# Kernel optimization log

Measured on AMD Instinct MI355X. Metric: run time of the kernel, lower is better.

Reference implementation:

```python
import jax, jax.numpy as jnp
import numpy as np

B, S, HN, TN = 8, 32, 64, 512
HID, EMB, VOCAB = 512, 512, 10000


def setup_inputs():
    key = jax.random.key(0)
    k = jax.random.split(key, 14)
    w = lambda kk, shape: jax.random.normal(kk, shape, jnp.float32) * 0.02
    return {
        "dec_out": jax.random.normal(k[0], (B, S, HID), jnp.float32),
        "history": jax.random.normal(k[1], (B, HID), jnp.float32),
        "head": jax.random.randint(k[2], (B, HN), 0, VOCAB),
        "tail": jax.random.randint(k[3], (B, TN), 0, VOCAB),
        "adj_mask": jax.random.randint(k[4], (B, HN, TN), 0, 2).astype(bool),
        "dup_mask": jax.random.randint(k[5], (B, S, TN), 0, 2).astype(bool),
        "emb_table": w(k[6], (VOCAB, EMB)),
        "W_tq": w(k[7], (2 * HID + EMB, HID)),
        "b_tq": jnp.zeros((HID,), jnp.float32),
        "W_tk": w(k[8], (EMB, HID)),
        "b_tk": jnp.zeros((HID,), jnp.float32),
        "W_tout": w(k[9], (2 * HID, HID)),
        "W_hq": w(k[10], (2 * HID, HID)),
        "b_hq": jnp.zeros((HID,), jnp.float32),
        "W_hk": w(k[11], (HID, HID)),
        "b_hk": jnp.zeros((HID,), jnp.float32),
    }


def reference(dec_out, history, head, tail, adj_mask, dup_mask, emb_table,
              W_tq, b_tq, W_tk, b_tk, W_tout, W_hq, b_hq, W_hk, b_hk):
    head_emb = emb_table[head]  # (B, HN, EMB)
    tail_emb = emb_table[tail]  # (B, TN, EMB)

    # --- tail attention query: Linear(cat([dec_out, history, head_emb])) + ELU.
    # Same math as the torch broadcast-concat, computed as a sum of three
    # partial matmuls to avoid materializing the (B,S,HN,2*hid+emb) concat.
    Wd, Wh, We = W_tq[:HID], W_tq[HID:2 * HID], W_tq[2 * HID:]
    tq = jax.nn.elu((dec_out @ Wd)[:, :, None, :]
                    + (history @ Wh)[:, None, None, :]
                    + (head_emb @ We)[:, None, :, :]
                    + b_tq)                       # (B, S, HN, HID)
    tq = tq.reshape(B, S * HN, HID)
    tk = jax.nn.elu(tail_emb @ W_tk + b_tk)       # (B, TN, HID)  (dropout=eval)

    # combined logical mask: allowed = adjacency AND not-duplicate
    mask = (adj_mask[:, None, :, :] & ~dup_mask[:, :, None, :]).reshape(B, S * HN, TN)

    # GlobalAttention (dot): score -> mask -> softmax -> context -> tanh(linear_out([c;q]))
    scores = jnp.einsum('bqh,bth->bqt', tq, tk)   # (B, S*HN, TN)
    tail_attn = jax.nn.softmax(jnp.where(mask, scores, -jnp.inf), axis=-1)
    ctx = jnp.einsum('bqt,bth->bqh', tail_attn, tk)
    graph_hid = jnp.tanh(ctx @ W_tout[:HID] + tq @ W_tout[HID:])
    graph_hid = graph_hid.reshape(B * S, HN, HID)
    tail_attn = tail_attn.reshape(B * S, HN, TN)

    # --- head attention (one-step), length-masked over HN
    hq = jax.nn.elu(dec_out @ W_hq[:HID] + (history @ W_hq[HID:])[:, None, :] + b_hq)
    hq = hq.reshape(B * S, HID)
    hk = jax.nn.elu(jnp.einsum('nkh,hd->nkd', graph_hid, W_hk) + b_hk)
    lengths = jnp.repeat(jnp.sum(head != 0, axis=-1), S)          # (B*S,)
    hscores = jnp.einsum('nh,nkh->nk', hq, hk)                    # (B*S, HN)
    lmask = jnp.arange(HN)[None, :] < lengths[:, None]
    head_attn = jax.nn.softmax(jnp.where(lmask, hscores, -jnp.inf), axis=-1)
    # (head-attention context output is discarded by the original module)

    prob = jnp.einsum('nk,nkt->nt', head_attn, tail_attn).reshape(B, S, TN)
    return jnp.log(prob + 1e-20)
```

## Files before the change

kernel.cpp:

```cpp
#include <hip/hip_runtime.h>
#include <math.h>

#define BB 8
#define SS 32
#define HN 64
#define TN 512
#define HID 512

typedef __attribute__((ext_vector_type(8))) short short8;
typedef __attribute__((ext_vector_type(4))) float f32x4;

__device__ __forceinline__ float eluf(float x) { return x > 0.f ? x : (expf(x) - 1.f); }

__device__ __forceinline__ short f2bs(float f) {
    union { float f; unsigned int u; } v; v.f = f;
    unsigned int r = v.u + 0x7fffu + ((v.u >> 16) & 1u);
    return (short)(r >> 16);
}
__device__ __forceinline__ float b2f(short s) {
    union { unsigned int u; float f; } v;
    v.u = ((unsigned int)(unsigned short)s) << 16;
    return v.f;
}

__device__ __forceinline__ void gld16(const void* g, void* l) {
    __builtin_amdgcn_global_load_lds(
        (const __attribute__((address_space(1))) void*)g,
        (__attribute__((address_space(3))) void*)l, 16, 0, 0);
}

template <int ACT, int OUTB, int DUAL>
__device__ __forceinline__ void gcore(
    const short* __restrict__ A, const short* __restrict__ B,
    const short* __restrict__ A2, const short* __restrict__ B2,
    const float* __restrict__ bias, void* __restrict__ Cv,
    int ldc, int K, int m0, int n0, int cm0, short* Ls,
    const float* __restrict__ hq, float* __restrict__ hsp)
{
    short* Al = Ls;
    short* Bl = Ls + 8192;
    const int tid  = threadIdx.x;
    const int lane = tid & 63;
    const int w    = tid >> 6;
    const int wr   = w >> 1, wc = w & 1;
    const int l16  = lane & 15, quad = lane >> 4;

    const int srow = w * 16 + (lane >> 2);
    const int scol = (lane & 3) * 8;

    f32x4 acc[4][4];
#pragma unroll
    for (int i = 0; i < 4; ++i)
#pragma unroll
        for (int j = 0; j < 4; ++j) { acc[i][j][0]=0.f; acc[i][j][1]=0.f; acc[i][j][2]=0.f; acc[i][j][3]=0.f; }

    short* lA = Al + w * 512;
    short* lB = Bl + w * 512;
    const long rstep = (long)64 * K;

    for (int rep = 0; rep <= DUAL; ++rep) {
        const short* Ag = (rep ? A2 : A) + (long)(m0 + srow) * K + scol;
        const short* Bg = (rep ? B2 : B) + (long)(n0 + srow) * K + scol;
        for (int kt = 0; kt < K; kt += 64) {
            __syncthreads();
            gld16(Ag + kt, lA);
            gld16(Ag + kt + rstep, lA + 2048);
            gld16(Ag + kt + 32, lA + 4096);
            gld16(Ag + kt + 32 + rstep, lA + 4096 + 2048);
            gld16(Bg + kt, lB);
            gld16(Bg + kt + rstep, lB + 2048);
            gld16(Bg + kt + 32, lB + 4096);
            gld16(Bg + kt + 32 + rstep, lB + 4096 + 2048);
            __syncthreads();
#pragma unroll
            for (int h = 0; h < 2; ++h) {
                short8 af[4], bf4[4];
#pragma unroll
                for (int mi = 0; mi < 4; ++mi)
                    af[mi] = *(const short8*)(Al + h * 4096 + (wr * 64 + mi * 16 + l16) * 32 + quad * 8);
#pragma unroll
                for (int ni = 0; ni < 4; ++ni)
                    bf4[ni] = *(const short8*)(Bl + h * 4096 + (wc * 64 + ni * 16 + l16) * 32 + quad * 8);
#pragma unroll
                for (int mi = 0; mi < 4; ++mi)
#pragma unroll
                    for (int ni = 0; ni < 4; ++ni)
                        acc[mi][ni] = __builtin_amdgcn_mfma_f32_16x16x32_bf16(af[mi], bf4[ni], acc[mi][ni], 0, 0, 0);
            }
        }
    }

    __syncthreads();

    float bv[4];
#pragma unroll
    for (int ni = 0; ni < 4; ++ni)
        bv[ni] = bias ? bias[n0 + wc * 64 + ni * 16 + l16] : 0.f;

    if (OUTB == 1) {
        short* eb = Ls + w * 1152;
        const int er = lane >> 2;
        const int ec = (lane & 3) * 16;
#pragma unroll
        for (int mi = 0; mi < 4; ++mi) {
#pragma unroll
            for (int ni = 0; ni < 4; ++ni)
#pragma unroll
                for (int r = 0; r < 4; ++r) {
                    float x = acc[mi][ni][r] + bv[ni];
                    if (ACT == 1) x = eluf(x);
                    else if (ACT == 2) x = tanhf(x);
                    eb[(quad * 4 + r) * 72 + ni * 16 + l16] = f2bs(x);
                }
            __builtin_amdgcn_sched_barrier(0);
            short8 v0 = *(const short8*)&eb[er * 72 + ec];
            short8 v1 = *(const short8*)&eb[er * 72 + ec + 8];
            long cb = (long)(cm0 + wr * 64 + mi * 16 + er) * ldc + n0 + wc * 64 + ec;
            *(short8*)((short*)Cv + cb)     = v0;
            *(short8*)((short*)Cv + cb + 8) = v1;
            __builtin_amdgcn_sched_barrier(0);
        }
    } else if (OUTB == 2) {
        const int n_w = (cm0 + wr * 64) >> 6;
        float hqv[4];
#pragma unroll
        for (int ni = 0; ni < 4; ++ni)
            hqv[ni] = hq[(long)n_w * 512 + n0 + wc * 64 + ni * 16 + l16];
        float* red = (float*)Ls;
#pragma unroll
        for (int mi = 0; mi < 4; ++mi)
#pragma unroll
            for (int r = 0; r < 4; ++r) {
                float p = 0.f;
#pragma unroll
                for (int ni = 0; ni < 4; ++ni) {
                    float x = acc[mi][ni][r] + bv[ni];
                    if (ACT == 1) x = eluf(x);
                    p += x * hqv[ni];
                }
                p += __shfl_xor(p, 1);
                p += __shfl_xor(p, 2);
                p += __shfl_xor(p, 4);
                p += __shfl_xor(p, 8);
                if (l16 == 0) red[w * 64 + mi * 16 + quad * 4 + r] = p;
            }
        __syncthreads();
        if (tid < 128) {
            int wr2 = tid >> 6, rw = tid & 63;
            float v = red[(wr2 * 2 + 0) * 64 + rw] + red[(wr2 * 2 + 1) * 64 + rw];
            hsp[(long)(n0 >> 7) * 16384 + cm0 + tid] = v;
        }
    } else {
#pragma unroll
        for (int mi = 0; mi < 4; ++mi)
#pragma unroll
            for (int ni = 0; ni < 4; ++ni) {
                int gc = n0 + wc * 64 + ni * 16 + l16;
#pragma unroll
                for (int r = 0; r < 4; ++r) {
                    float x = acc[mi][ni][r] + bv[ni];
                    if (ACT == 1) x = eluf(x);
                    else if (ACT == 2) x = tanhf(x);
                    ((float*)Cv)[(long)(cm0 + wr * 64 + mi * 16 + quad * 4 + r) * ldc + gc] = x;
                }
            }
    }
}

template <int ACT, int OUTB, int DUAL>
__global__ __launch_bounds__(256) void mgemm(
    const short* __restrict__ A, long sAz,
    const short* __restrict__ B, long sBz,
    const short* __restrict__ A2, long sA2z,
    const short* __restrict__ B2,
    const float* __restrict__ bias,
    void* __restrict__ Cv, long sCz, int ldc, int K)
{
    __shared__ short Ls[16384];
    const int z = blockIdx.z;
    void* C = OUTB ? (void*)((short*)Cv + (long)z * sCz) : (void*)((float*)Cv + (long)z * sCz);
    const short* A2z = DUAL ? (A2 + (long)z * sA2z) : nullptr;
    gcore<ACT, OUTB, DUAL>(A + (long)z * sAz, B + (long)z * sBz, A2z, B2, bias, C,
                           ldc, K, blockIdx.y * 128, blockIdx.x * 128, blockIdx.y * 128, Ls,
                           nullptr, nullptr);
}

__global__ __launch_bounds__(256) void mgemm_hs(
    const short* __restrict__ A, const short* __restrict__ B,
    const float* __restrict__ bias, const float* __restrict__ hq, float* __restrict__ hsp)
{
    __shared__ short Ls[16384];
    gcore<1, 2, 0>(A, B, nullptr, nullptr, bias, nullptr, 512, 512,
                   blockIdx.y * 128, blockIdx.x * 128, blockIdx.y * 128, Ls, hq, hsp);
}

__global__ __launch_bounds__(256) void mgemm_multi(
    const short* __restrict__ decb, const short* __restrict__ WTall, float* __restrict__ qall,
    const short* __restrict__ embAll, const short* __restrict__ WTe, float* __restrict__ qe,
    const short* __restrict__ WTk, const float* __restrict__ b_tk, short* __restrict__ tkb)
{
    __shared__ short Ls[16384];
    int id = blockIdx.x;
    if (id < 48) {
        int y = id >> 4, x = id & 15;
        gcore<0, 0, 0>(decb, WTall, nullptr, nullptr, nullptr, qall, 2048, 512,
                       y * 128, x * 128, y * 128, Ls, nullptr, nullptr);
    } else if (id < 64) {
        int id2 = id - 48, y = id2 >> 2, x = id2 & 3;
        gcore<0, 0, 0>(embAll, WTe, nullptr, nullptr, nullptr, qe, 512, 512,
                       y * 128, x * 128, y * 128, Ls, nullptr, nullptr);
    } else {
        int id3 = id - 64, y = id3 >> 2, x = id3 & 3;
        gcore<1, 1, 0>(embAll, WTk, nullptr, nullptr, b_tk, tkb, 512, 512,
                       512 + y * 128, x * 128, y * 128, Ls, nullptr, nullptr);
    }
}

struct WTDesc { const float* src[9]; short* dst[9]; };

__global__ __launch_bounds__(256) void prep(
    const float* __restrict__ dec_out, const float* __restrict__ history,
    short* __restrict__ decb,
    const float* __restrict__ emb, const int* __restrict__ head, const int* __restrict__ tail,
    short* __restrict__ embAll, WTDesc wd)
{
    __shared__ float t[32][33];
    const int id = blockIdx.x, tid = threadIdx.x;
    if (id < 528) {
        int i = id * 256 + tid;
        float v = (i < 131072) ? dec_out[i] : history[i - 131072];
        decb[i] = f2bs(v);
    } else if (id < 528 + 4608) {
        int r = id - 528;
        int idx = (r < 512) ? head[r] : tail[r - 512];
        const float* s = emb + (long)idx * 512;
        short* dst = embAll + (long)r * 512;
        dst[tid]       = f2bs(s[tid]);
        dst[tid + 256] = f2bs(s[tid + 256]);
    } else {
        int q = id - 5136;
        int z = q >> 8, xy = q & 255;
        int x = xy & 15, y = xy >> 4;
        const float* src = wd.src[z];
        short* dst = wd.dst[z];
        int k0 = y * 32, n0 = x * 32;
        int tx = tid & 31, ty = tid >> 5;
#pragma unroll
        for (int i = 0; i < 32; i += 8)
            t[ty + i][tx] = src[(long)(k0 + ty + i) * 512 + n0 + tx];
        __syncthreads();
#pragma unroll
        for (int i = 0; i < 32; i += 8)
            dst[(long)(n0 + ty + i) * 512 + k0 + tx] = f2bs(t[tx][ty + i]);
    }
}

__global__ __launch_bounds__(256) void l3_kernel(
    const float* __restrict__ qall, const float* __restrict__ qe,
    const float* __restrict__ b_tq, short* __restrict__ tqb,
    const short* __restrict__ WTo1, const short* __restrict__ tkb, short* __restrict__ tkWTb,
    const float* __restrict__ b_hq, float* __restrict__ hqf)
{
    __shared__ short Ls[16384];
    if (blockIdx.x < 8192) {
        long gid = (long)blockIdx.x * 256 + threadIdx.x;
        int r = (int)(gid >> 7), j0 = ((int)gid & 127) * 4;
        int b = r >> 11, rem = r & 2047, s = rem >> 6, h = rem & 63;
        float4 d = *(const float4*)(qall + (long)(b * 32 + s) * 2048 + j0);
        float4 q = *(const float4*)(qall + (long)(256 + b) * 2048 + 1024 + j0);
        float4 e = *(const float4*)(qe + (long)(b * 64 + h) * 512 + j0);
        float4 bb = *(const float4*)(b_tq + j0);
        short4 o;
        o.x = f2bs(eluf(d.x + q.x + e.x + bb.x));
        o.y = f2bs(eluf(d.y + q.y + e.y + bb.y));
        o.z = f2bs(eluf(d.z + q.z + e.z + bb.z));
        o.w = f2bs(eluf(d.w + q.w + e.w + bb.w));
        *(short4*)(tqb + (long)r * 512 + j0) = o;
    } else if (blockIdx.x < 8320) {
        int id2 = blockIdx.x - 8192;
        int z = id2 >> 4, r = id2 & 15;
        int x = r & 3, y = r >> 2;
        gcore<0, 1, 0>(WTo1, tkb + (long)z * 262144, nullptr, nullptr, nullptr,
                       tkWTb + (long)z * 262144, 512, 512, y * 128, x * 128, y * 128, Ls,
                       nullptr, nullptr);
    } else {
        long gid = (long)(blockIdx.x - 8320) * 256 + threadIdx.x;
        int n = (int)(gid >> 7), j0 = ((int)gid & 127) * 4;
        int b = n >> 5;
        float4 d = *(const float4*)(qall + (long)n * 2048 + 512 + j0);
        float4 h2 = *(const float4*)(qall + (long)(256 + b) * 2048 + 1536 + j0);
        float4 bb = *(const float4*)(b_hq + j0);
        float4 o;
        o.x = eluf(d.x + h2.x + bb.x);
        o.y = eluf(d.y + h2.y + bb.y);
        o.z = eluf(d.z + h2.z + bb.z);
        o.w = eluf(d.w + h2.w + bb.w);
        *(float4*)(hqf + (long)n * 512 + j0) = o;
    }
}

__global__ __launch_bounds__(256) void sm_kernel(
    const short* __restrict__ sc, const int* __restrict__ adj, const int* __restrict__ dup,
    short* __restrict__ Pb)
{
    int w = threadIdx.x >> 6, lane = threadIdx.x & 63;
    long r = (long)blockIdx.x * 4 + w;
    int b = (int)(r >> 11), rem = (int)(r & 2047), s = rem >> 6, h = rem & 63;
    const short* row = sc + r * 512 + lane * 8;
    const int* adjr = adj + ((long)(b * 64 + h)) * 512 + lane * 8;
    const int* dupr = dup + ((long)(b * 32 + s)) * 512 + lane * 8;
    short8 v8 = *(const short8*)row;
    int4 a0 = *(const int4*)adjr, a1 = *(const int4*)(adjr + 4);
    int4 d0 = *(const int4*)dupr, d1 = *(const int4*)(dupr + 4);
    int am[8] = {a0.x, a0.y, a0.z, a0.w, a1.x, a1.y, a1.z, a1.w};
    int dm[8] = {d0.x, d0.y, d0.z, d0.w, d1.x, d1.y, d1.z, d1.w};
    float v[8];
    float m = -INFINITY;
#pragma unroll
    for (int i = 0; i < 8; ++i) {
        v[i] = (am[i] && !dm[i]) ? b2f(v8[i]) : -INFINITY;
        m = fmaxf(m, v[i]);
    }
#pragma unroll
    for (int d = 32; d >= 1; d >>= 1) m = fmaxf(m, __shfl_xor(m, d));
    float sum = 0.f;
#pragma unroll
    for (int i = 0; i < 8; ++i) {
        float e = (m == -INFINITY) ? 0.f : expf(v[i] - m);
        v[i] = e; sum += e;
    }
#pragma unroll
    for (int d = 32; d >= 1; d >>= 1) sum += __shfl_xor(sum, d);
    float inv = sum > 0.f ? 1.f / sum : 0.f;
    short8 o;
#pragma unroll
    for (int i = 0; i < 8; ++i) o[i] = f2bs(v[i] * inv);
    *(short8*)(Pb + r * 512 + lane * 8) = o;
}

__global__ __launch_bounds__(256) void fused_head(
    const float* __restrict__ hsp, const int* __restrict__ head,
    const short* __restrict__ ta, float* __restrict__ out)
{
    int n = blockIdx.x, b = n >> 5;
    int tid = threadIdx.x;
    __shared__ float hal[64];
    __shared__ float part[4][512];

    if (tid < 64) {
        float sv_raw = hsp[n * 64 + tid] + hsp[16384 + n * 64 + tid]
                     + hsp[2 * 16384 + n * 64 + tid] + hsp[3 * 16384 + n * 64 + tid];
        int hv = head[b * 64 + tid];
        unsigned long long ball = __ballot(hv != 0);
        int len = __popcll(ball);
        float sv = (tid < len) ? sv_raw : -INFINITY;
        float m = sv;
#pragma unroll
        for (int d = 32; d >= 1; d >>= 1) m = fmaxf(m, __shfl_xor(m, d));
        float e = expf(sv - m);
        float sum = e;
#pragma unroll
        for (int d = 32; d >= 1; d >>= 1) sum += __shfl_xor(sum, d);
        hal[tid] = e / sum;
    }
    __syncthreads();

    {
        int w = tid >> 6, lane = tid & 63;
        const short* tab = ta + (long)n * 64 * 512 + (long)(w * 16) * 512 + lane * 8;
        float acc[8] = {};
#pragma unroll
        for (int k = 0; k < 16; ++k) {
            float a = hal[w * 16 + k];
            short8 tv = *(const short8*)(tab + (long)k * 512);
#pragma unroll
            for (int u = 0; u < 8; ++u) acc[u] += a * b2f(tv[u]);
        }
        float4* pp = (float4*)&part[w][lane * 8];
        pp[0] = make_float4(acc[0], acc[1], acc[2], acc[3]);
        pp[1] = make_float4(acc[4], acc[5], acc[6], acc[7]);
    }
    __syncthreads();

    for (int t = tid; t < 512; t += 256) {
        float a = part[0][t] + part[1][t] + part[2][t] + part[3][t];
        out[(long)n * 512 + t] = logf(a + 1e-20f);
    }
}

extern "C" void kernel_launch(void* const* d_in, const int* in_sizes, int n_in,
                              void* d_out, int out_size, void* d_ws, size_t ws_size,
                              hipStream_t stream)
{
    const float* dec_out = (const float*)d_in[0];
    const float* history = (const float*)d_in[1];
    const int*   head    = (const int*)d_in[2];
    const int*   tail    = (const int*)d_in[3];
    const int*   adj     = (const int*)d_in[4];
    const int*   dup     = (const int*)d_in[5];
    const float* emb     = (const float*)d_in[6];
    const float* W_tq    = (const float*)d_in[7];
    const float* b_tq    = (const float*)d_in[8];
    const float* W_tk    = (const float*)d_in[9];
    const float* b_tk    = (const float*)d_in[10];
    const float* W_tout  = (const float*)d_in[11];
    const float* W_hq    = (const float*)d_in[12];
    const float* b_hq    = (const float*)d_in[13];
    const float* W_hk    = (const float*)d_in[14];
    const float* b_hk    = (const float*)d_in[15];
    float* out = (float*)d_out;

    char* ws = (char*)d_ws;
    auto alloc = [&](size_t bytes) -> void* {
        char* p = ws;
        ws += (bytes + 255) & ~(size_t)255;
        return (void*)p;
    };
    short* decb   = (short*)alloc((size_t)384 * 512 * 2);
    short* embAll = (short*)alloc((size_t)4608 * 512 * 2);
    short* WT     = (short*)alloc((size_t)9 * 512 * 512 * 2);
    float* qall   = (float*)alloc((size_t)384 * 2048 * 4);
    float* qe     = (float*)alloc((size_t)512 * 512 * 4);
    float* hqf    = (float*)alloc((size_t)256 * 512 * 4);
    float* hsp    = (float*)alloc((size_t)4 * 16384 * 4);
    short* tkb    = (short*)alloc((size_t)4096 * 512 * 2);
    short* tkWTb  = (short*)alloc((size_t)4096 * 512 * 2);
    short* tqb    = (short*)alloc((size_t)16384 * 512 * 2);
    short* scb    = (short*)alloc((size_t)16384 * 512 * 2);
    short* Pb     = (short*)alloc((size_t)16384 * 512 * 2);
    short* ghb = scb;

    WTDesc wd;
    wd.src[0] = W_tq;               wd.dst[0] = WT;
    wd.src[1] = W_hq;               wd.dst[1] = WT + (size_t)1 * 262144;
    wd.src[2] = W_tq + 512 * 512;   wd.dst[2] = WT + (size_t)2 * 262144;
    wd.src[3] = W_hq + 512 * 512;   wd.dst[3] = WT + (size_t)3 * 262144;
    wd.src[4] = W_tq + 1024 * 512;  wd.dst[4] = WT + (size_t)4 * 262144;
    wd.src[5] = W_tk;               wd.dst[5] = WT + (size_t)5 * 262144;
    wd.src[6] = W_tout;             wd.dst[6] = WT + (size_t)6 * 262144;
    wd.src[7] = W_tout + 512 * 512; wd.dst[7] = WT + (size_t)7 * 262144;
    wd.src[8] = W_hk;               wd.dst[8] = WT + (size_t)8 * 262144;

    prep<<<7440, 256, 0, stream>>>(dec_out, history, decb, emb, head, tail, embAll, wd);
    mgemm_multi<<<192, 256, 0, stream>>>(decb, WT, qall, embAll, WT + (size_t)4 * 262144, qe,
                                         WT + (size_t)5 * 262144, b_tk, tkb);
    l3_kernel<<<8448, 256, 0, stream>>>(qall, qe, b_tq, tqb, WT + (size_t)6 * 262144, tkb, tkWTb,
                                        b_hq, hqf);
    mgemm<0, 1, 0><<<dim3(4, 16, 8), 256, 0, stream>>>(
        tqb, (long)2048 * 512, tkb, 262144, nullptr, 0, nullptr, nullptr,
        scb, (long)2048 * 512, 512, 512);
    sm_kernel<<<4096, 256, 0, stream>>>(scb, adj, dup, Pb);
    mgemm<2, 1, 1><<<dim3(4, 16, 8), 256, 0, stream>>>(
        Pb, (long)2048 * 512, tkWTb, 262144, tqb, (long)2048 * 512, WT + (size_t)7 * 262144,
        nullptr, ghb, (long)2048 * 512, 512, 512);
    mgemm_hs<<<dim3(4, 128), 256, 0, stream>>>(ghb, WT + (size_t)8 * 262144, b_hk, hqf, hsp);
    fused_head<<<256, 256, 0, stream>>>(hsp, head, Pb, out);
}
```

Measured before the change: 224.4 us.

## Shrink GEMM tiles to 64x128 with two-wave blocks to double grid size

The shared GEMM core changes from a 128x128 tile computed by four waves to a 64x128 tile computed by two waves, each wave owning a 64x64 sub-tile. Block size drops to 128 threads, LDS use drops to 24KB, and every GEMM launch grid doubles, along with the element-wise part of l3_kernel. The goal is more blocks and better CU occupancy on the small GEMMs (e.g. 192 or 512 blocks on a large GPU). In exchange, B-tile reuse per block falls and global loads per FLOP rise.

Result: slower. 238.2 us (+6.2%).

```diff
diff --git a/kernel.cpp b/kernel.cpp
--- a/kernel.cpp
+++ b/kernel.cpp
@@ -30,7 +30,7 @@
 }
 
 template <int ACT, int OUTB, int DUAL>
-__device__ __forceinline__ void gcore(
+__device__ __forceinline__ void gcore2(
     const short* __restrict__ A, const short* __restrict__ B,
     const short* __restrict__ A2, const short* __restrict__ B2,
     const float* __restrict__ bias, void* __restrict__ Cv,
@@ -38,11 +38,10 @@
     const float* __restrict__ hq, float* __restrict__ hsp)
 {
     short* Al = Ls;
-    short* Bl = Ls + 8192;
+    short* Bl = Ls + 4096;
     const int tid  = threadIdx.x;
     const int lane = tid & 63;
     const int w    = tid >> 6;
-    const int wr   = w >> 1, wc = w & 1;
     const int l16  = lane & 15, quad = lane >> 4;
 
     const int srow = w * 16 + (lane >> 2);
@@ -54,33 +53,36 @@
 #pragma unroll
         for (int j = 0; j < 4; ++j) { acc[i][j][0]=0.f; acc[i][j][1]=0.f; acc[i][j][2]=0.f; acc[i][j][3]=0.f; }
 
-    short* lA = Al + w * 512;
-    short* lB = Bl + w * 512;
-    const long rstep = (long)64 * K;
+    const int wb = w * 16;
+    const long r32 = (long)32 * K;
 
     for (int rep = 0; rep <= DUAL; ++rep) {
         const short* Ag = (rep ? A2 : A) + (long)(m0 + srow) * K + scol;
         const short* Bg = (rep ? B2 : B) + (long)(n0 + srow) * K + scol;
         for (int kt = 0; kt < K; kt += 64) {
             __syncthreads();
-            gld16(Ag + kt, lA);
-            gld16(Ag + kt + rstep, lA + 2048);
-            gld16(Ag + kt + 32, lA + 4096);
-            gld16(Ag + kt + 32 + rstep, lA + 4096 + 2048);
-            gld16(Bg + kt, lB);
-            gld16(Bg + kt + rstep, lB + 2048);
-            gld16(Bg + kt + 32, lB + 4096);
-            gld16(Bg + kt + 32 + rstep, lB + 4096 + 2048);
+            gld16(Ag + kt,            Al + (wb) * 32);
+            gld16(Ag + kt + r32,      Al + (wb + 32) * 32);
+            gld16(Ag + kt + 32,       Al + 2048 + (wb) * 32);
+            gld16(Ag + kt + r32 + 32, Al + 2048 + (wb + 32) * 32);
+            gld16(Bg + kt,                Bl + (wb) * 32);
+            gld16(Bg + kt + r32,          Bl + (wb + 32) * 32);
+            gld16(Bg + kt + 2 * r32,      Bl + (wb + 64) * 32);
+            gld16(Bg + kt + 3 * r32,      Bl + (wb + 96) * 32);
+            gld16(Bg + kt + 32,           Bl + 4096 + (wb) * 32);
+            gld16(Bg + kt + r32 + 32,     Bl + 4096 + (wb + 32) * 32);
+            gld16(Bg + kt + 2 * r32 + 32, Bl + 4096 + (wb + 64) * 32);
+            gld16(Bg + kt + 3 * r32 + 32, Bl + 4096 + (wb + 96) * 32);
             __syncthreads();
 #pragma unroll
             for (int h = 0; h < 2; ++h) {
                 short8 af[4], bf4[4];
 #pragma unroll
                 for (int mi = 0; mi < 4; ++mi)
-                    af[mi] = *(const short8*)(Al + h * 4096 + (wr * 64 + mi * 16 + l16) * 32 + quad * 8);
+                    af[mi] = *(const short8*)(Al + h * 2048 + (mi * 16 + l16) * 32 + quad * 8);
 #pragma unroll
                 for (int ni = 0; ni < 4; ++ni)
-                    bf4[ni] = *(const short8*)(Bl + h * 4096 + (wc * 64 + ni * 16 + l16) * 32 + quad * 8);
+                    bf4[ni] = *(const short8*)(Bl + h * 4096 + (w * 64 + ni * 16 + l16) * 32 + quad * 8);
 #pragma unroll
                 for (int mi = 0; mi < 4; ++mi)
 #pragma unroll
@@ -95,7 +97,7 @@
     float bv[4];
 #pragma unroll
     for (int ni = 0; ni < 4; ++ni)
-        bv[ni] = bias ? bias[n0 + wc * 64 + ni * 16 + l16] : 0.f;
+        bv[ni] = bias ? bias[n0 + w * 64 + ni * 16 + l16] : 0.f;
 
     if (OUTB == 1) {
         short* eb = Ls + w * 1152;
@@ -115,17 +117,17 @@
             __builtin_amdgcn_sched_barrier(0);
             short8 v0 = *(const short8*)&eb[er * 72 + ec];
             short8 v1 = *(const short8*)&eb[er * 72 + ec + 8];
-            long cb = (long)(cm0 + wr * 64 + mi * 16 + er) * ldc + n0 + wc * 64 + ec;
+            long cb = (long)(cm0 + mi * 16 + er) * ldc + n0 + w * 64 + ec;
             *(short8*)((short*)Cv + cb)     = v0;
             *(short8*)((short*)Cv + cb + 8) = v1;
             __builtin_amdgcn_sched_barrier(0);
         }
     } else if (OUTB == 2) {
-        const int n_w = (cm0 + wr * 64) >> 6;
+        const int n_w = cm0 >> 6;
         float hqv[4];
 #pragma unroll
         for (int ni = 0; ni < 4; ++ni)
-            hqv[ni] = hq[(long)n_w * 512 + n0 + wc * 64 + ni * 16 + l16];
+            hqv[ni] = hq[(long)n_w * 512 + n0 + w * 64 + ni * 16 + l16];
         float* red = (float*)Ls;
 #pragma unroll
         for (int mi = 0; mi < 4; ++mi)
@@ -145,30 +147,27 @@
                 if (l16 == 0) red[w * 64 + mi * 16 + quad * 4 + r] = p;
             }
         __syncthreads();
-        if (tid < 128) {
-            int wr2 = tid >> 6, rw = tid & 63;
-            float v = red[(wr2 * 2 + 0) * 64 + rw] + red[(wr2 * 2 + 1) * 64 + rw];
-            hsp[(long)(n0 >> 7) * 16384 + cm0 + tid] = v;
-        }
+        if (tid < 64)
+            hsp[(long)(n0 >> 7) * 16384 + cm0 + tid] = red[tid] + red[64 + tid];
     } else {
 #pragma unroll
         for (int mi = 0; mi < 4; ++mi)
 #pragma unroll
             for (int ni = 0; ni < 4; ++ni) {
-                int gc = n0 + wc * 64 + ni * 16 + l16;
+                int gc = n0 + w * 64 + ni * 16 + l16;
 #pragma unroll
                 for (int r = 0; r < 4; ++r) {
                     float x = acc[mi][ni][r] + bv[ni];
                     if (ACT == 1) x = eluf(x);
                     else if (ACT == 2) x = tanhf(x);
-                    ((float*)Cv)[(long)(cm0 + wr * 64 + mi * 16 + quad * 4 + r) * ldc + gc] = x;
+                    ((float*)Cv)[(long)(cm0 + mi * 16 + quad * 4 + r) * ldc + gc] = x;
                 }
             }
     }
 }
 
 template <int ACT, int OUTB, int DUAL>
-__global__ __launch_bounds__(256) void mgemm(
+__global__ __launch_bounds__(128) void mgemm(
     const short* __restrict__ A, long sAz,
     const short* __restrict__ B, long sBz,
     const short* __restrict__ A2, long sA2z,
@@ -176,43 +175,43 @@
     const float* __restrict__ bias,
     void* __restrict__ Cv, long sCz, int ldc, int K)
 {
-    __shared__ short Ls[16384];
+    __shared__ short Ls[12288];
     const int z = blockIdx.z;
     void* C = OUTB ? (void*)((short*)Cv + (long)z * sCz) : (void*)((float*)Cv + (long)z * sCz);
     const short* A2z = DUAL ? (A2 + (long)z * sA2z) : nullptr;
-    gcore<ACT, OUTB, DUAL>(A + (long)z * sAz, B + (long)z * sBz, A2z, B2, bias, C,
-                           ldc, K, blockIdx.y * 128, blockIdx.x * 128, blockIdx.y * 128, Ls,
-                           nullptr, nullptr);
-}
-
-__global__ __launch_bounds__(256) void mgemm_hs(
+    gcore2<ACT, OUTB, DUAL>(A + (long)z * sAz, B + (long)z * sBz, A2z, B2, bias, C,
+                            ldc, K, blockIdx.y * 64, blockIdx.x * 128, blockIdx.y * 64, Ls,
+                            nullptr, nullptr);
+}
+
+__global__ __launch_bounds__(128) void mgemm_hs(
     const short* __restrict__ A, const short* __restrict__ B,
     const float* __restrict__ bias, const float* __restrict__ hq, float* __restrict__ hsp)
 {
-    __shared__ short Ls[16384];
-    gcore<1, 2, 0>(A, B, nullptr, nullptr, bias, nullptr, 512, 512,
-                   blockIdx.y * 128, blockIdx.x * 128, blockIdx.y * 128, Ls, hq, hsp);
-}
-
-__global__ __launch_bounds__(256) void mgemm_multi(
+    __shared__ short Ls[12288];
+    gcore2<1, 2, 0>(A, B, nullptr, nullptr, bias, nullptr, 512, 512,
+                    blockIdx.y * 64, blockIdx.x * 128, blockIdx.y * 64, Ls, hq, hsp);
+}
+
+__global__ __launch_bounds__(128) void mgemm_multi(
     const short* __restrict__ decb, const short* __restrict__ WTall, float* __restrict__ qall,
     const short* __restrict__ embAll, const short* __restrict__ WTe, float* __restrict__ qe,
     const short* __restrict__ WTk, const float* __restrict__ b_tk, short* __restrict__ tkb)
 {
-    __shared__ short Ls[16384];
+    __shared__ short Ls[12288];
     int id = blockIdx.x;
-    if (id < 48) {
+    if (id < 96) {
         int y = id >> 4, x = id & 15;
-        gcore<0, 0, 0>(decb, WTall, nullptr, nullptr, nullptr, qall, 2048, 512,
-                       y * 128, x * 128, y * 128, Ls, nullptr, nullptr);
-    } else if (id < 64) {
-        int id2 = id - 48, y = id2 >> 2, x = id2 & 3;
-        gcore<0, 0, 0>(embAll, WTe, nullptr, nullptr, nullptr, qe, 512, 512,
-                       y * 128, x * 128, y * 128, Ls, nullptr, nullptr);
+        gcore2<0, 0, 0>(decb, WTall, nullptr, nullptr, nullptr, qall, 2048, 512,
+                        y * 64, x * 128, y * 64, Ls, nullptr, nullptr);
+    } else if (id < 128) {
+        int id2 = id - 96, y = id2 >> 2, x = id2 & 3;
+        gcore2<0, 0, 0>(embAll, WTe, nullptr, nullptr, nullptr, qe, 512, 512,
+                        y * 64, x * 128, y * 64, Ls, nullptr, nullptr);
     } else {
-        int id3 = id - 64, y = id3 >> 2, x = id3 & 3;
-        gcore<1, 1, 0>(embAll, WTk, nullptr, nullptr, b_tk, tkb, 512, 512,
-                       512 + y * 128, x * 128, y * 128, Ls, nullptr, nullptr);
+        int id3 = id - 128, y = id3 >> 2, x = id3 & 3;
+        gcore2<1, 1, 0>(embAll, WTk, nullptr, nullptr, b_tk, tkb, 512, 512,
+                        512 + y * 64, x * 128, y * 64, Ls, nullptr, nullptr);
     }
 }
 
@@ -255,15 +254,15 @@
     }
 }
 
-__global__ __launch_bounds__(256) void l3_kernel(
+__global__ __launch_bounds__(128) void l3_kernel(
     const float* __restrict__ qall, const float* __restrict__ qe,
     const float* __restrict__ b_tq, short* __restrict__ tqb,
     const short* __restrict__ WTo1, const short* __restrict__ tkb, short* __restrict__ tkWTb,
     const float* __restrict__ b_hq, float* __restrict__ hqf)
 {
-    __shared__ short Ls[16384];
-    if (blockIdx.x < 8192) {
-        long gid = (long)blockIdx.x * 256 + threadIdx.x;
+    __shared__ short Ls[12288];
+    if (blockIdx.x < 16384) {
+        long gid = (long)blockIdx.x * 128 + threadIdx.x;
         int r = (int)(gid >> 7), j0 = ((int)gid & 127) * 4;
         int b = r >> 11, rem = r & 2047, s = rem >> 6, h = rem & 63;
         float4 d = *(const float4*)(qall + (long)(b * 32 + s) * 2048 + j0);
@@ -276,15 +275,15 @@
         o.z = f2bs(eluf(d.z + q.z + e.z + bb.z));
         o.w = f2bs(eluf(d.w + q.w + e.w + bb.w));
         *(short4*)(tqb + (long)r * 512 + j0) = o;
-    } else if (blockIdx.x < 8320) {
-        int id2 = blockIdx.x - 8192;
-        int z = id2 >> 4, r = id2 & 15;
+    } else if (blockIdx.x < 16640) {
+        int id2 = blockIdx.x - 16384;
+        int z = id2 >> 5, r = id2 & 31;
         int x = r & 3, y = r >> 2;
-        gcore<0, 1, 0>(WTo1, tkb + (long)z * 262144, nullptr, nullptr, nullptr,
-                       tkWTb + (long)z * 262144, 512, 512, y * 128, x * 128, y * 128, Ls,
-                       nullptr, nullptr);
+        gcore2<0, 1, 0>(WTo1, tkb + (long)z * 262144, nullptr, nullptr, nullptr,
+                        tkWTb + (long)z * 262144, 512, 512, y * 64, x * 128, y * 64, Ls,
+                        nullptr, nullptr);
     } else {
-        long gid = (long)(blockIdx.x - 8320) * 256 + threadIdx.x;
+        long gid = (long)(blockIdx.x - 16640) * 128 + threadIdx.x;
         int n = (int)(gid >> 7), j0 = ((int)gid & 127) * 4;
         int b = n >> 5;
         float4 d = *(const float4*)(qall + (long)n * 2048 + 512 + j0);
@@ -442,17 +441,17 @@
     wd.src[8] = W_hk;               wd.dst[8] = WT + (size_t)8 * 262144;
 
     prep<<<7440, 256, 0, stream>>>(dec_out, history, decb, emb, head, tail, embAll, wd);
-    mgemm_multi<<<192, 256, 0, stream>>>(decb, WT, qall, embAll, WT + (size_t)4 * 262144, qe,
+    mgemm_multi<<<384, 128, 0, stream>>>(decb, WT, qall, embAll, WT + (size_t)4 * 262144, qe,
                                          WT + (size_t)5 * 262144, b_tk, tkb);
-    l3_kernel<<<8448, 256, 0, stream>>>(qall, qe, b_tq, tqb, WT + (size_t)6 * 262144, tkb, tkWTb,
-                                        b_hq, hqf);
-    mgemm<0, 1, 0><<<dim3(4, 16, 8), 256, 0, stream>>>(
+    l3_kernel<<<16896, 128, 0, stream>>>(qall, qe, b_tq, tqb, WT + (size_t)6 * 262144, tkb, tkWTb,
+                                         b_hq, hqf);
+    mgemm<0, 1, 0><<<dim3(4, 32, 8), 128, 0, stream>>>(
         tqb, (long)2048 * 512, tkb, 262144, nullptr, 0, nullptr, nullptr,
         scb, (long)2048 * 512, 512, 512);
     sm_kernel<<<4096, 256, 0, stream>>>(scb, adj, dup, Pb);
-    mgemm<2, 1, 1><<<dim3(4, 16, 8), 256, 0, stream>>>(
+    mgemm<2, 1, 1><<<dim3(4, 32, 8), 128, 0, stream>>>(
         Pb, (long)2048 * 512, tkWTb, 262144, tqb, (long)2048 * 512, WT + (size_t)7 * 262144,
         nullptr, ghb, (long)2048 * 512, 512, 512);
-    mgemm_hs<<<dim3(4, 128), 256, 0, stream>>>(ghb, WT + (size_t)8 * 262144, b_hk, hqf, hsp);
+    mgemm_hs<<<dim3(4, 256), 128, 0, stream>>>(ghb, WT + (size_t)8 * 262144, b_hk, hqf, hsp);
     fused_head<<<256, 256, 0, stream>>>(hsp, head, Pb, out);
 }
```
